# Optimization experiments

Measured on AMD Instinct MI355X. Metric: run time of the kernel, lower is better.

## Reference

```python
import jax, jax.numpy as jnp
import numpy as np

C = 256
R = 4

def setup_inputs() -> dict:
    key = jax.random.key(0)
    k_x, k1, k2, k3, kb = jax.random.split(key, 5)
    B, H, W = 32, 128, 128
    Cr = C // R
    x = jax.random.normal(k_x, (B, C, H, W), dtype=jnp.float32)
    # torch nn.Linear weights: (out_features, in_features)
    W1 = jax.random.normal(k1, (Cr, C), dtype=jnp.float32) * (1.0 / np.sqrt(C))
    W2 = jax.random.normal(k2, (C, Cr), dtype=jnp.float32) * (1.0 / np.sqrt(Cr))
    W3 = jax.random.normal(k3, (2, C), dtype=jnp.float32) * (1.0 / np.sqrt(C))
    b3 = jax.random.normal(kb, (2,), dtype=jnp.float32) * (1.0 / np.sqrt(C))
    return {"x": x, "W1": W1, "W2": W2, "W3": W3, "b3": b3}

def reference(x, W1, W2, W3, b3):
    # f = global avg pool -> (B, C)
    f = jnp.mean(x, axis=(2, 3))
    f = jax.nn.relu(f @ W1.T)            # (B, C//r)
    f = jax.nn.sigmoid(f @ W2.T)         # (B, C)
    # scale full tensor by per-channel gate, then avg-pool again (faithful to source)
    scale = x * f[:, :, None, None]      # (B, C, H, W)
    p = jnp.mean(scale, axis=(2, 3))     # (B, C)
    return p @ W3.T + b3                 # (B, 2)
```

## Files before the change

kernel.cpp:

```cpp
#include <hip/hip_runtime.h>
#include <hip/hip_bf16.h>
#include <math.h>


#define HW 16384
#define C 256
#define CR 64
#define B 32

__global__ __launch_bounds__(256) void pool_kernel(const float* __restrict__ x,
                                                   float* __restrict__ f0) {
    const int plane = blockIdx.x;
    const float4* p = (const float4*)(x + (size_t)plane * HW);
    const int tid = threadIdx.x;
    float s = 0.f;
#pragma unroll
    for (int i = 0; i < 16; ++i) {
        float4 v = p[i * 256 + tid];
        s += (v.x + v.y) + (v.z + v.w);
    }
#pragma unroll
    for (int off = 32; off > 0; off >>= 1) s += __shfl_down(s, off, 64);
    __shared__ float ws[4];
    if ((tid & 63) == 0) ws[tid >> 6] = s;
    __syncthreads();
    if (tid == 0) {
        f0[plane] = (ws[0] + ws[1] + ws[2] + ws[3]) * (1.0f / (float)HW);
    }
}

__global__ __launch_bounds__(256) void mlp_kernel(const float* __restrict__ f0,
                                                  const float* __restrict__ W1,
                                                  const float* __restrict__ W2,
                                                  const float* __restrict__ W3,
                                                  const float* __restrict__ b3,
                                                  float* __restrict__ out) {
    const int b = blockIdx.x;
    const int tid = threadIdx.x;
    __shared__ float f0s[C];
    __shared__ float f1s[CR];
    __shared__ float ps[C];
    __shared__ float red[2][4];

    f0s[tid] = f0[b * C + tid];
    __syncthreads();

    if (tid < CR) {
        const float* w = W1 + tid * C;
        float acc = 0.f;
#pragma unroll 8
        for (int i = 0; i < C; ++i) acc = fmaf(f0s[i], w[i], acc);
        f1s[tid] = fmaxf(acc, 0.f);
    }
    __syncthreads();

    {
        const float* w = W2 + tid * CR;
        float acc = 0.f;
#pragma unroll
        for (int i = 0; i < CR; ++i) acc = fmaf(f1s[i], w[i], acc);
        float g = 1.0f / (1.0f + expf(-acc));
        ps[tid] = g * f0s[tid];
    }
    __syncthreads();

#pragma unroll
    for (int o = 0; o < 2; ++o) {
        float v = ps[tid] * W3[o * C + tid];
#pragma unroll
        for (int off = 32; off > 0; off >>= 1) v += __shfl_down(v, off, 64);
        if ((tid & 63) == 0) red[o][tid >> 6] = v;
    }
    __syncthreads();
    if (tid < 2) {
        out[b * 2 + tid] = red[tid][0] + red[tid][1] + red[tid][2] + red[tid][3] + b3[tid];
    }
}

extern "C" void kernel_launch(void* const* d_in, const int* in_sizes, int n_in,
                              void* d_out, int out_size, void* d_ws, size_t ws_size,
                              hipStream_t stream) {
    const float* x  = (const float*)d_in[0];
    const float* W1 = (const float*)d_in[1];
    const float* W2 = (const float*)d_in[2];
    const float* W3 = (const float*)d_in[3];
    const float* b3 = (const float*)d_in[4];
    float* out = (float*)d_out;
    float* f0  = (float*)d_ws;

    pool_kernel<<<B * C, 256, 0, stream>>>(x, f0);
    mlp_kernel<<<B, 256, 0, stream>>>(f0, W1, W2, W3, b3, out);
}
```

Measured before the change: 686.7 us.

## Fuse pooling and MLP into one kernel via last-block atomic counter

```diff
diff --git a/kernel.cpp b/kernel.cpp
--- a/kernel.cpp
+++ b/kernel.cpp
@@ -7,73 +7,89 @@
 #define C 256
 #define CR 64
 #define B 32
+#define NPLANE (B * C)
 
-__global__ __launch_bounds__(256) void pool_kernel(const float* __restrict__ x,
-                                                   float* __restrict__ f0) {
+
+__global__ __launch_bounds__(256) void fused_kernel(const float* __restrict__ x,
+                                                    const float* __restrict__ W1,
+                                                    const float* __restrict__ W2,
+                                                    const float* __restrict__ W3,
+                                                    const float* __restrict__ b3,
+                                                    float* __restrict__ out,
+                                                    float* __restrict__ f0,
+                                                    int* __restrict__ counter) {
     const int plane = blockIdx.x;
-    const float4* p = (const float4*)(x + (size_t)plane * HW);
     const int tid = threadIdx.x;
-    float s = 0.f;
+    __shared__ float ws[4];
+
+    {
+        const float4* p = (const float4*)(x + (size_t)plane * HW);
+        float s = 0.f;
 #pragma unroll
-    for (int i = 0; i < 16; ++i) {
-        float4 v = p[i * 256 + tid];
-        s += (v.x + v.y) + (v.z + v.w);
+        for (int i = 0; i < 16; ++i) {
+            float4 v = p[i * 256 + tid];
+            s += (v.x + v.y) + (v.z + v.w);
+        }
+#pragma unroll
+        for (int off = 32; off > 0; off >>= 1) s += __shfl_down(s, off, 64);
+        if ((tid & 63) == 0) ws[tid >> 6] = s;
+        __syncthreads();
+        if (tid == 0) {
+            f0[plane] = (ws[0] + ws[1] + ws[2] + ws[3]) * (1.0f / (float)HW);
+        }
     }
-#pragma unroll
-    for (int off = 32; off > 0; off >>= 1) s += __shfl_down(s, off, 64);
-    __shared__ float ws[4];
-    if ((tid & 63) == 0) ws[tid >> 6] = s;
+
+    __shared__ int is_last;
+    __threadfence();
+    if (tid == 0) {
+        int old = atomicAdd(counter, 1);
+        is_last = (old == NPLANE - 1) ? 1 : 0;
+    }
     __syncthreads();
-    if (tid == 0) {
-        f0[plane] = (ws[0] + ws[1] + ws[2] + ws[3]) * (1.0f / (float)HW);
-    }
-}
+    if (!is_last) return;
+    __threadfence();
 
-__global__ __launch_bounds__(256) void mlp_kernel(const float* __restrict__ f0,
-                                                  const float* __restrict__ W1,
-                                                  const float* __restrict__ W2,
-                                                  const float* __restrict__ W3,
-                                                  const float* __restrict__ b3,
-                                                  float* __restrict__ out) {
-    const int b = blockIdx.x;
-    const int tid = threadIdx.x;
     __shared__ float f0s[C];
     __shared__ float f1s[CR];
     __shared__ float ps[C];
     __shared__ float red[2][4];
 
-    f0s[tid] = f0[b * C + tid];
-    __syncthreads();
+    for (int b = 0; b < B; ++b) {
+        f0s[tid] = f0[b * C + tid];
+        __syncthreads();
 
-    if (tid < CR) {
-        const float* w = W1 + tid * C;
-        float acc = 0.f;
+        if (tid < CR) {
+            const float* w = W1 + tid * C;
+            float acc = 0.f;
 #pragma unroll 8
-        for (int i = 0; i < C; ++i) acc = fmaf(f0s[i], w[i], acc);
-        f1s[tid] = fmaxf(acc, 0.f);
-    }
-    __syncthreads();
+            for (int i = 0; i < C; ++i) acc = fmaf(f0s[i], w[i], acc);
+            f1s[tid] = fmaxf(acc, 0.f);
+        }
+        __syncthreads();
 
-    {
-        const float* w = W2 + tid * CR;
-        float acc = 0.f;
+        {
+            const float* w = W2 + tid * CR;
+            float acc = 0.f;
 #pragma unroll
-        for (int i = 0; i < CR; ++i) acc = fmaf(f1s[i], w[i], acc);
-        float g = 1.0f / (1.0f + expf(-acc));
-        ps[tid] = g * f0s[tid];
-    }
-    __syncthreads();
+            for (int i = 0; i < CR; ++i) acc = fmaf(f1s[i], w[i], acc);
+            float g = 1.0f / (1.0f + expf(-acc));
+            ps[tid] = g * f0s[tid];
+        }
+        __syncthreads();
 
 #pragma unroll
-    for (int o = 0; o < 2; ++o) {
-        float v = ps[tid] * W3[o * C + tid];
+        for (int o = 0; o < 2; ++o) {
+            float v = ps[tid] * W3[o * C + tid];
 #pragma unroll
-        for (int off = 32; off > 0; off >>= 1) v += __shfl_down(v, off, 64);
-        if ((tid & 63) == 0) red[o][tid >> 6] = v;
-    }
-    __syncthreads();
-    if (tid < 2) {
-        out[b * 2 + tid] = red[tid][0] + red[tid][1] + red[tid][2] + red[tid][3] + b3[tid];
+            for (int off = 32; off > 0; off >>= 1) v += __shfl_down(v, off, 64);
+            if ((tid & 63) == 0) red[o][tid >> 6] = v;
+        }
+        __syncthreads();
+        if (tid < 2) {
+            out[b * 2 + tid] =
+                red[tid][0] + red[tid][1] + red[tid][2] + red[tid][3] + b3[tid];
+        }
+        __syncthreads();
     }
 }
 
@@ -87,7 +103,9 @@
     const float* b3 = (const float*)d_in[4];
     float* out = (float*)d_out;
     float* f0  = (float*)d_ws;
+    int* counter = (int*)((char*)d_ws + NPLANE * sizeof(float));
 
-    pool_kernel<<<B * C, 256, 0, stream>>>(x, f0);
-    mlp_kernel<<<B, 256, 0, stream>>>(f0, W1, W2, W3, b3, out);
+    hipMemsetAsync(counter, 0, sizeof(int), stream);
+
+    fused_kernel<<<NPLANE, 256, 0, stream>>>(x, W1, W2, W3, b3, out, f0, counter);
 }
```

Result: slower. 2.563 ms (+273.2%).
